# Kernel tuning notes

Hardware: AMD Instinct MI355X
Metric: run time of the kernel (lower is better)

Reference implementation:

```python
import jax, jax.numpy as jnp
import numpy as np

WS = 7            # cubic window
HEADS = 6
DIM = 96          # attention channel dim (concat of two half-streams)
CH = 48           # per-stream channels (dim // 2)
HID = 384         # int(dim * mlp_ratio)
N = WS ** 3       # 343 tokens per window
EPS = 1e-5


def _rel_pos_index():
    c = np.stack(np.meshgrid(np.arange(WS), np.arange(WS), np.arange(WS), indexing='ij')).reshape(3, -1)
    rel = (c[:, :, None] - c[:, None, :]).transpose(1, 2, 0) + (WS - 1)
    rel[:, :, 0] *= (2 * WS - 1) * (2 * WS - 1)
    rel[:, :, 1] *= (2 * WS - 1)
    return rel.sum(-1)  # (N, N) int

RPI = jnp.asarray(_rel_pos_index())


def _ln(x, g, b):
    m = x.mean(-1, keepdims=True)
    v = ((x - m) ** 2).mean(-1, keepdims=True)
    return (x - m) * jax.lax.rsqrt(v + EPS) * g + b


def _win_part(x):
    B, H, W, T, C = x.shape
    x = x.reshape(B, H // WS, WS, W // WS, WS, T // WS, WS, C)
    return x.transpose(0, 1, 3, 5, 2, 4, 6, 7).reshape(-1, WS, WS, WS, C)


def _win_rev(w, B, H, W, T):
    C = w.shape[-1]
    x = w.reshape(B, H // WS, W // WS, T // WS, WS, WS, WS, C)
    return x.transpose(0, 1, 4, 2, 5, 3, 6, 7).reshape(B, H, W, T, C)


def _chessboard(wa, wb, gd, gh, gw):
    C = wa.shape[-1]
    a = wa.reshape(gd, gh, gw, WS, WS, WS, C)
    b = wb.reshape(gd, gh, gw, WS, WS, WS, C)
    i = jnp.arange(gd)[:, None, None]
    j = jnp.arange(gh)[None, :, None]
    k = jnp.arange(gw)[None, None, :]
    m = (((i + j + k) % 2) == 0)[..., None, None, None, None]
    return (jnp.where(m, a, b).reshape(-1, WS, WS, WS, C),
            jnp.where(m, b, a).reshape(-1, WS, WS, WS, C))


def _attn(x, mask, rpb, qkv_w, qkv_b, proj_w, proj_b):
    B_, n, C = x.shape
    hd = C // HEADS
    qkv = (x @ qkv_w + qkv_b).reshape(B_, n, 3, HEADS, hd).transpose(2, 0, 3, 1, 4)
    q, k, v = qkv[0] * (hd ** -0.5), qkv[1], qkv[2]
    att = jnp.einsum('bhnd,bhmd->bhnm', q, k)
    att = att + rpb[RPI].transpose(2, 0, 1)[None]   # relative position bias gather
    att = att + mask[:, None]                        # shift mask; B_ == nW since B == 1
    att = jax.nn.softmax(att, axis=-1)
    out = jnp.einsum('bhnm,bhmd->bhnd', att, v).transpose(0, 2, 1, 3).reshape(B_, n, C)
    return out @ proj_w + proj_b


def _mlp(x, w1, b1, w2, b2):
    return jax.nn.gelu(x @ w1 + b1, approximate=False) @ w2 + b2


def _forward(x_a, x_b, mask_matrix, n1a_g, n1a_b, n1b_g, n1b_b,
             rpb_a, qkvw_a, qkvb_a, projw_a, projb_a,
             rpb_b, qkvw_b, qkvb_b, projw_b, projb_b,
             n2a_g, n2a_b, n2b_g, n2b_b,
             fc1w_a, fc1b_a, fc2w_a, fc2b_a, fc1w_b, fc1b_b, fc2w_b, fc2b_b,
             gw1, gw2, gb2, H, W, T):
    B, L, _ = x_a.shape
    sa0, sb0 = x_a, x_b
    a = _ln(x_a, n1a_g, n1a_b).reshape(B, H, W, T, CH)
    b = _ln(x_b, n1b_g, n1b_b).reshape(B, H, W, T, CH)
    # chessboard cross-stream shuffle of windows (shifted-window branch)
    ca, cb = _chessboard(_win_part(a), _win_part(b), H // WS, W // WS, T // WS)
    a_cr = _win_rev(ca, B, H, W, T)
    b_cr = _win_rev(cb, B, H, W, T)
    neg, pos, dims = (-3, -3, -3), (3, 3, 3), (1, 2, 3)
    sa, sb = jnp.roll(a, neg, dims), jnp.roll(b, neg, dims)
    sac, sbc = jnp.roll(a_cr, neg, dims), jnp.roll(b_cr, neg, dims)
    xa_w = _win_part(jnp.concatenate([sa, sbc], -1)).reshape(-1, N, DIM)
    xb_w = _win_part(jnp.concatenate([sb, sac], -1)).reshape(-1, N, DIM)
    oa = _attn(xa_w, mask_matrix, rpb_a, qkvw_a, qkvb_a, projw_a, projb_a)
    ob = _attn(xb_w, mask_matrix, rpb_b, qkvw_b, qkvb_b, projw_b, projb_b)
    oa = jnp.roll(_win_rev(oa.reshape(-1, WS, WS, WS, DIM), B, H, W, T), pos, dims)[..., :CH].reshape(B, L, CH)
    ob = jnp.roll(_win_rev(ob.reshape(-1, WS, WS, WS, DIM), B, H, W, T), pos, dims)[..., :CH].reshape(B, L, CH)
    x_a = sa0 + oa
    x_b = sb0 + ob
    x_a = x_a + _mlp(_ln(x_a, n2a_g, n2a_b), fc1w_a, fc1b_a, fc2w_a, fc2b_a)
    x_b = x_b + _mlp(_ln(x_b, n2b_g, n2b_b), fc1w_b, fc1b_b, fc2w_b, fc2b_b)
    g = jax.nn.sigmoid(jnp.maximum(x_a.mean(1) @ gw1, 0.0) @ gw2 + gb2)[:, :, None]  # (B,1,1)
    x_a = x_a + g * x_b
    return x_a, x_b


def setup_inputs():
    key = jax.random.key(0)
    ks = iter(jax.random.split(key, 24))
    H = W = T = 35
    L = H * W * T
    nW = (H // WS) * (W // WS) * (T // WS)
    p = lambda shape: jax.random.normal(next(ks), shape, jnp.float32) * 0.02
    d = {
        'x_a': jax.random.normal(next(ks), (1, L, CH), jnp.float32),
        'x_b': jax.random.normal(next(ks), (1, L, CH), jnp.float32),
        'mask_matrix': jax.random.normal(next(ks), (nW, N, N), jnp.float32),
        'n1a_g': jnp.ones((CH,), jnp.float32), 'n1a_b': jnp.zeros((CH,), jnp.float32),
        'n1b_g': jnp.ones((CH,), jnp.float32), 'n1b_b': jnp.zeros((CH,), jnp.float32),
        'rpb_a': p(((2 * WS - 1) ** 3, HEADS)),
        'qkvw_a': p((DIM, 3 * DIM)), 'qkvb_a': jnp.zeros((3 * DIM,), jnp.float32),
        'projw_a': p((DIM, DIM)), 'projb_a': jnp.zeros((DIM,), jnp.float32),
        'rpb_b': p(((2 * WS - 1) ** 3, HEADS)),
        'qkvw_b': p((DIM, 3 * DIM)), 'qkvb_b': jnp.zeros((3 * DIM,), jnp.float32),
        'projw_b': p((DIM, DIM)), 'projb_b': jnp.zeros((DIM,), jnp.float32),
        'n2a_g': jnp.ones((CH,), jnp.float32), 'n2a_b': jnp.zeros((CH,), jnp.float32),
        'n2b_g': jnp.ones((CH,), jnp.float32), 'n2b_b': jnp.zeros((CH,), jnp.float32),
        'fc1w_a': p((CH, HID)), 'fc1b_a': jnp.zeros((HID,), jnp.float32),
        'fc2w_a': p((HID, CH)), 'fc2b_a': jnp.zeros((CH,), jnp.float32),
        'fc1w_b': p((CH, HID)), 'fc1b_b': jnp.zeros((HID,), jnp.float32),
        'fc2w_b': p((HID, CH)), 'fc2b_b': jnp.zeros((CH,), jnp.float32),
        'gw1': p((CH, CH // 4)), 'gw2': p((CH // 4, 1)),
        'gb2': jnp.full((1,), -2.0, jnp.float32),
        'H': H, 'W': W, 'T': T,
    }
    return d


def reference(x_a, x_b, mask_matrix, n1a_g, n1a_b, n1b_g, n1b_b,
              rpb_a, qkvw_a, qkvb_a, projw_a, projb_a,
              rpb_b, qkvw_b, qkvb_b, projw_b, projb_b,
              n2a_g, n2a_b, n2b_g, n2b_b,
              fc1w_a, fc1b_a, fc2w_a, fc2b_a, fc1w_b, fc1b_b, fc2w_b, fc2b_b,
              gw1, gw2, gb2, H, W, T):
    return _forward(x_a, x_b, mask_matrix, n1a_g, n1a_b, n1b_g, n1b_b,
                    rpb_a, qkvw_a, qkvb_a, projw_a, projb_a,
                    rpb_b, qkvw_b, qkvb_b, projw_b, projb_b,
                    n2a_g, n2a_b, n2b_g, n2b_b,
                    fc1w_a, fc1b_a, fc2w_a, fc2b_a, fc1w_b, fc1b_b, fc2w_b, fc2b_b,
                    gw1, gw2, gb2, H, W, T)
```

## Files before the change

kernel.cpp:

```cpp
#include <hip/hip_runtime.h>
#include <hip/hip_fp16.h>

#define LQ    42875
#define NTOK  343
#define X1SZ  2058000

#define OFF_MEAN 0
#define OFF_QKV  36928
#define OFF_WF   12500000
#define QKV_BYTES_NEEDED 50400000ull

typedef _Float16 f16x8 __attribute__((ext_vector_type(8)));
typedef float f32x4 __attribute__((ext_vector_type(4)));
union B128 { uint4 u; f16x8 h; _Float16 e[8]; };

__device__ __forceinline__ int src_index(int w, int i, int& par) {
  int gi = w / 25, gj = (w / 5) % 5, gk = w % 5;
  int ph = i / 49, pw = (i / 7) % 7, pt = i % 7;
  int hs = gi * 7 + ph + 3; if (hs >= 35) hs -= 35;
  int wd = gj * 7 + pw + 3; if (wd >= 35) wd -= 35;
  int td = gk * 7 + pt + 3; if (td >= 35) td -= 35;
  par = ((hs / 7) + (wd / 7) + (td / 7)) & 1;
  return (hs * 35 + wd) * 35 + td;
}

__global__ __launch_bounds__(64) void k_init(float* __restrict__ ws) {
  if (threadIdx.x < 49) ws[threadIdx.x] = 0.f;
}

__global__ __launch_bounds__(256) void k_pack(
    const float* __restrict__ w1a, const float* __restrict__ w1b,
    const float* __restrict__ w2a, const float* __restrict__ w2b,
    const float* __restrict__ qwa, const float* __restrict__ qwb,
    float* __restrict__ ws) {
  int idx = blockIdx.x * 256 + threadIdx.x;
  if (idx >= 17664) return;
  uint4* WFB = (uint4*)(ws + OFF_WF);
  unsigned short h[8];
  uint4* dst;
  if (idx < 10752) {
    int s = idx / 5376, r = idx - s * 5376;
    uint4* WF = WFB + (size_t)s * 5376;
    if (r < 3072) {
      int jn = r / 128, t = r - jn * 128, kk = t / 64, lane = t - kk * 64;
      int q = lane >> 4, n = lane & 15;
      const float* w1 = s ? w1b : w1a;
      int j = jn * 16 + n;
#pragma unroll
      for (int e = 0; e < 8; e++) {
        int k = kk * 32 + q * 8 + e;
        float v = (k < 48) ? w1[k * 384 + j] : 0.f;
        h[e] = __half_as_ushort(__float2half(v));
      }
    } else {
      int rr = r - 3072;
      int kt = rr / 192, t = rr - kt * 192, cn = t / 64, lane = t - cn * 64;
      int q = lane >> 4, n = lane & 15;
      const float* w2 = s ? w2b : w2a;
      int c = cn * 16 + n;
#pragma unroll
      for (int e = 0; e < 8; e++) {
        int j = kt * 32 + q * 8 + e;
        h[e] = __half_as_ushort(__float2half(w2[j * 48 + c]));
      }
    }
    dst = WF + r;
  } else {
    int idx2 = idx - 10752;
    int s = idx2 / 3456, r = idx2 - s * 3456;
    int jn = r / 192, t = r - jn * 192, kk = t / 64, lane = t - kk * 64;
    int q = lane >> 4, n = lane & 15;
    const float* qw = s ? qwb : qwa;
    int j = jn * 16 + n;
#pragma unroll
    for (int e = 0; e < 8; e++) {
      int k = kk * 32 + q * 8 + e;
      h[e] = __half_as_ushort(__float2half(qw[k * 288 + j]));
    }
    dst = WFB + 10752 + (size_t)s * 3456 + r;
  }
  uint4 u;
  u.x = (unsigned)h[0] | ((unsigned)h[1] << 16);
  u.y = (unsigned)h[2] | ((unsigned)h[3] << 16);
  u.z = (unsigned)h[4] | ((unsigned)h[5] << 16);
  u.w = (unsigned)h[6] | ((unsigned)h[7] << 16);
  *dst = u;
}

__global__ __launch_bounds__(256) void k_qkv(
    const float* __restrict__ xa, const float* __restrict__ xb,
    const float* __restrict__ ga, const float* __restrict__ ba,
    const float* __restrict__ gb, const float* __restrict__ bb,
    const float* __restrict__ qba, const float* __restrict__ qbb,
    const float* __restrict__ ws, __half* __restrict__ qkvh) {
  __shared__ uint4 LDSB[2368];
  int s = blockIdx.z;
  int tid = threadIdx.x;
  int wid = tid >> 6, lane = tid & 63;
  int quad = lane >> 4, n15 = lane & 15;
  uint4* WR = LDSB + wid * 592;
  _Float16* th = (_Float16*)WR;
  int tbase = blockIdx.x * 64 + wid * 16;

  if (lane < 32) {
    int tt = lane & 15, which = lane >> 4;
    int t = tbase + tt;
    float v[48];
    bool wr = false, dup = false;
    if (t < LQ) {
      int w = t / 343, i = t - w * 343;
      int par; int src = src_index(w, i, par);
      const float* xr; const float* G; const float* B;
      bool doit;
      if (which == 0) { xr = (s ? xb : xa) + src * 48; G = s ? gb : ga; B = s ? bb : ba; doit = true; dup = (par == 1); }
      else            { xr = (s ? xa : xb) + src * 48; G = s ? ga : gb; B = s ? ba : bb; doit = (par == 0); }
      if (doit) {
        float sm = 0.f, sq = 0.f;
#pragma unroll
        for (int q4 = 0; q4 < 12; q4++) {
          float4 tv = ((const float4*)xr)[q4];
          v[4 * q4] = tv.x; v[4 * q4 + 1] = tv.y; v[4 * q4 + 2] = tv.z; v[4 * q4 + 3] = tv.w;
          sm += tv.x + tv.y + tv.z + tv.w;
          sq += tv.x * tv.x + tv.y * tv.y + tv.z * tv.z + tv.w * tv.w;
        }
        float m = sm * (1.f / 48.f);
        float r = rsqrtf(sq * (1.f / 48.f) - m * m + 1e-5f);
#pragma unroll
        for (int k = 0; k < 48; k++) v[k] = (v[k] - m) * r * G[k] + B[k];
        wr = true;
      }
    } else if (which == 0) {
#pragma unroll
      for (int k = 0; k < 48; k++) v[k] = 0.f;
      wr = true; dup = true;
    }
    if (wr) {
#pragma unroll
      for (int c6 = 0; c6 < 6; c6++) {
        unsigned short h[8];
#pragma unroll
        for (int e = 0; e < 8; e++) h[e] = __half_as_ushort(__float2half(v[c6 * 8 + e]));
        uint4 u;
        u.x = (unsigned)h[0] | ((unsigned)h[1] << 16);
        u.y = (unsigned)h[2] | ((unsigned)h[3] << 16);
        u.z = (unsigned)h[4] | ((unsigned)h[5] << 16);
        u.w = (unsigned)h[6] | ((unsigned)h[7] << 16);
        WR[(which * 6 + c6) * 16 + tt] = u;
        if (dup) WR[(6 + c6) * 16 + tt] = u;
      }
    }
  }

  B128 ax0, ax1, ax2;
  ax0.u = WR[(0 + quad) * 16 + n15];
  ax1.u = WR[(4 + quad) * 16 + n15];
  ax2.u = WR[(8 + quad) * 16 + n15];

  const uint4* QF = (const uint4*)(ws + OFF_WF) + 10752 + (size_t)s * 3456;
  const float* QB = s ? qbb : qba;
  const f32x4 ZC = {0.f, 0.f, 0.f, 0.f};

  for (int jn = 0; jn < 18; jn++) {
    B128 b0, b1, b2;
    b0.u = QF[(jn * 3 + 0) * 64 + lane];
    b1.u = QF[(jn * 3 + 1) * 64 + lane];
    b2.u = QF[(jn * 3 + 2) * 64 + lane];
    f32x4 c = __builtin_amdgcn_mfma_f32_16x16x32_f16(ax0.h, b0.h, ZC, 0, 0, 0);
    c = __builtin_amdgcn_mfma_f32_16x16x32_f16(ax1.h, b1.h, c, 0, 0, 0);
    c = __builtin_amdgcn_mfma_f32_16x16x32_f16(ax2.h, b2.h, c, 0, 0, 0);
    float bias = QB[jn * 16 + n15];
    float scale = (jn < 6) ? 0.25f : 1.0f;
#pragma unroll
    for (int r = 0; r < 4; r++)
      th[(quad * 4 + r) * 296 + jn * 16 + n15] = (_Float16)((c[r] + bias) * scale);
  }
  for (int e = lane; e < 576; e += 64) {
    int row = e / 36, cc = e - row * 36;
    int t = tbase + row;
    if (t < LQ)
      ((uint4*)qkvh)[(size_t)(s * LQ + t) * 36 + cc] = WR[row * 37 + cc];
  }
}

__global__ __launch_bounds__(256) void k_attn(
    const float* __restrict__ rpa, const float* __restrict__ rpbp,
    const float* __restrict__ mask, __half* __restrict__ qkvh) {
  int bid = blockIdx.x;
  int xcd = bid & 7, q8 = bid >> 3;
  int u = q8 / 12, inst = q8 - u * 12;
  int w = u * 8 + xcd;
  if (w >= 125) return;
  int s = inst & 1, h = inst >> 1;

  __shared__ uint4 FRAG[2368];
  __shared__ float rpbl[2197];
  uint4* Qf4 = FRAG;
  uint4* Kf4 = FRAG + 704;
  uint4* Vf4 = FRAG + 1408;
  uint4* Pb4 = FRAG + 2112;
  _Float16* Vfh = (_Float16*)(FRAG + 1408);
  _Float16* Pbh = (_Float16*)(FRAG + 2112);

  int tid = threadIdx.x;
  const uint4 Z4 = {0u, 0u, 0u, 0u};
  for (int e = tid; e < 2112; e += 256) FRAG[e] = Z4;
  const float* rp = s ? rpbp : rpa;
  for (int idx = tid; idx < 2197; idx += 256) rpbl[idx] = rp[idx * 6 + h];
  __syncthreads();

  size_t wbase = (size_t)((s * 125 + w) * NTOK) * 288;
  for (int i = tid; i < NTOK; i += 256) {
    const uint4* row = (const uint4*)(qkvh + wbase + (size_t)i * 288) + (h * 2);
    uint4 q0 = row[0], q1 = row[1];
    uint4 k0 = row[12], k1 = row[13];
    B128 v0, v1; v0.u = row[24]; v1.u = row[25];
    int n = i & 15, it = i >> 4;
    Qf4[it * 32 + n] = q0;
    Qf4[it * 32 + 16 + n] = q1;
    Kf4[it * 32 + n] = k0;
    Kf4[it * 32 + 16 + n] = k1;
    int vbase = ((i >> 5) * 64 + ((i >> 3) & 3) * 16) * 8 + (i & 7);
#pragma unroll
    for (int d = 0; d < 8; d++) {
      Vfh[vbase + d * 8] = v0.e[d];
      Vfh[vbase + (d + 8) * 8] = v1.e[d];
    }
  }
  __syncthreads();

  int wid = tid >> 6, lane = tid & 63;
  int quad = lane >> 4, n15 = lane & 15;
  const f32x4 ZC = {0.f, 0.f, 0.f, 0.f};
  __half* obh = qkvh;

  for (int it = wid; it < 22; it += 4) {
    int i0 = it * 16;
    const float* mr[4]; int basei[4];
#pragma unroll
    for (int r = 0; r < 4; r++) {
      int ir = i0 + quad * 4 + r; if (ir > 342) ir = 342;
      mr[r] = mask + (size_t)(w * NTOK + ir) * NTOK;
      basei[r] = (ir / 49) * 169 + ((ir / 7) % 7) * 13 + (ir % 7) + 1098;
    }
    B128 qbits; qbits.u = Qf4[it * 32 + ((quad & 1) << 4) + n15];
    if (quad >= 2) qbits.u = Z4;
    f32x4 acc = ZC;
    float ls[4] = {0.f, 0.f, 0.f, 0.f};

    float mcur[8], mnxt[8];
    {
      int ja = n15, jb = n15 + 16;
#pragma unroll
      for (int r = 0; r < 4; r++) { mcur[r] = mr[r][ja]; mcur[4 + r] = mr[r][jb]; }
    }
    for (int j32 = 0; j32 < 11; j32++) {
      if (j32 < 10) {
        int ja = (j32 + 1) * 32 + n15, jb = ja + 16;
        bool vb = jb < NTOK;
#pragma unroll
        for (int r = 0; r < 4; r++) {
          mnxt[r] = mr[r][ja];
          mnxt[4 + r] = vb ? mr[r][jb] : -1e30f;
        }
      }
      B128 kb0, kb1;
      kb0.u = Kf4[(j32 * 2) * 32 + ((quad & 1) << 4) + n15];
      kb1.u = Kf4[(j32 * 2 + 1) * 32 + ((quad & 1) << 4) + n15];
      if (quad >= 2) { kb0.u = Z4; kb1.u = Z4; }
      f32x4 s0 = __builtin_amdgcn_mfma_f32_16x16x32_f16(qbits.h, kb0.h, ZC, 0, 0, 0);
      f32x4 s1 = __builtin_amdgcn_mfma_f32_16x16x32_f16(qbits.h, kb1.h, ZC, 0, 0, 0);
      int j0 = j32 * 32 + n15;
      int j1 = j0 + 16;
      int bj0 = (j0 / 49) * 169 + ((j0 / 7) % 7) * 13 + (j0 % 7);
      int bj1 = (j1 < 343) ? (j1 / 49) * 169 + ((j1 / 7) % 7) * 13 + (j1 % 7) : 0;
      float p0[4], p1[4];
#pragma unroll
      for (int r = 0; r < 4; r++) {
        float b0 = mcur[r] + rpbl[basei[r] - bj0];
        float b1 = mcur[4 + r] + rpbl[basei[r] - bj1];
        p0[r] = __expf(s0[r] + b0);
        p1[r] = __expf(s1[r] + b1);
        ls[r] += p0[r] + p1[r];
      }
      int jj = n15 & 7;
      int ldA = ((n15 >> 3) * 16 + quad * 4) * 8 + jj + wid * 512;
      int ldB = ((2 + (n15 >> 3)) * 16 + quad * 4) * 8 + jj + wid * 512;
#pragma unroll
      for (int r = 0; r < 4; r++) {
        Pbh[ldA + r * 8] = (_Float16)p0[r];
        Pbh[ldB + r * 8] = (_Float16)p1[r];
      }
      B128 pb, vbits;
      pb.u = Pb4[wid * 64 + lane];
      vbits.u = Vf4[j32 * 64 + lane];
      acc = __builtin_amdgcn_mfma_f32_16x16x32_f16(pb.h, vbits.h, acc, 0, 0, 0);
#pragma unroll
      for (int e = 0; e < 8; e++) mcur[e] = mnxt[e];
    }
#pragma unroll
    for (int r = 0; r < 4; r++) {
      float v = ls[r];
      v += __shfl_xor(v, 1); v += __shfl_xor(v, 2);
      v += __shfl_xor(v, 4); v += __shfl_xor(v, 8);
      int ir = i0 + quad * 4 + r;
      if (ir < 343)
        obh[wbase + (size_t)ir * 288 + h * 16 + n15] = __float2half(acc[r] * (1.f / v));
    }
  }
}

__global__ __launch_bounds__(384) void k_proj(
    const __half* __restrict__ qkvh,
    const float* __restrict__ xa0, const float* __restrict__ xb0,
    const float* __restrict__ pwa, const float* __restrict__ pba,
    const float* __restrict__ pwb, const float* __restrict__ pbb,
    float* __restrict__ out) {
  int sw = blockIdx.x; int s = sw / 125, w = sw - s * 125;
  int i = threadIdx.x;
  if (i >= NTOK) return;
  const float* Wt = s ? pwb : pwa;
  const float* Bi = s ? pbb : pba;
  const uint4* orow = (const uint4*)(qkvh + (size_t)((s * 125 + w) * NTOK + i) * 288);
  float acc[48];
#pragma unroll
  for (int c = 0; c < 48; c++) acc[c] = 0.f;
#pragma unroll
  for (int k8 = 0; k8 < 12; k8++) {
    B128 ov; ov.u = orow[k8];
#pragma unroll
    for (int e = 0; e < 8; e++) {
      float x = (float)ov.e[e];
      const float* wr = Wt + (k8 * 8 + e) * 96;
#pragma unroll
      for (int c = 0; c < 48; c++) acc[c] = fmaf(x, wr[c], acc[c]);
    }
  }
  int par; int src = src_index(w, i, par);
  const float* x0 = (s ? xb0 : xa0) + src * 48;
  float* dst = out + s * X1SZ + src * 48;
#pragma unroll
  for (int q = 0; q < 12; q++) {
    float4 xv = ((const float4*)x0)[q];
    float4 o;
    o.x = xv.x + acc[4 * q + 0] + Bi[4 * q + 0];
    o.y = xv.y + acc[4 * q + 1] + Bi[4 * q + 1];
    o.z = xv.z + acc[4 * q + 2] + Bi[4 * q + 2];
    o.w = xv.w + acc[4 * q + 3] + Bi[4 * q + 3];
    ((float4*)dst)[q] = o;
  }
}

__global__ __launch_bounds__(256) void k_mlp(
    const float* __restrict__ g2a, const float* __restrict__ b2a,
    const float* __restrict__ g2b, const float* __restrict__ b2b,
    const float* __restrict__ fb1a, const float* __restrict__ fb2a,
    const float* __restrict__ fb1b, const float* __restrict__ fb2b,
    float* __restrict__ out, float* __restrict__ ws) {
  __shared__ uint4 Xf[512];
  __shared__ uint4 tbu[320];
  __shared__ float red[48];
  int s = blockIdx.z;
  int tid = threadIdx.x;
  int wid = tid >> 6, lane = tid & 63;
  int quad = lane >> 4, n15 = lane & 15;
  if (tid < 48) red[tid] = 0.f;
  __syncthreads();

  const float* B1 = s ? fb1b : fb1a;
  const float* B2 = s ? fb2b : fb2a;
  const uint4* W1F = (const uint4*)(ws + OFF_WF) + (size_t)s * 5376;
  const uint4* W2F = W1F + 3072;
  int tbase = blockIdx.x * 64 + wid * 16;
  float* outs = out + (size_t)s * X1SZ;

  if (lane < 16) {
    int t = tbase + lane;
    float v[48];
    if (t < LQ) {
      const float* row = outs + (size_t)t * 48;
      float sm = 0.f, sq = 0.f;
#pragma unroll
      for (int q4 = 0; q4 < 12; q4++) {
        float4 tv = ((const float4*)row)[q4];
        v[4 * q4] = tv.x; v[4 * q4 + 1] = tv.y; v[4 * q4 + 2] = tv.z; v[4 * q4 + 3] = tv.w;
        sm += tv.x + tv.y + tv.z + tv.w;
        sq += tv.x * tv.x + tv.y * tv.y + tv.z * tv.z + tv.w * tv.w;
      }
      float m = sm * (1.f / 48.f);
      float r = rsqrtf(sq * (1.f / 48.f) - m * m + 1e-5f);
      const float* G = s ? g2b : g2a;
      const float* B = s ? b2b : b2a;
#pragma unroll
      for (int k = 0; k < 48; k++) v[k] = (v[k] - m) * r * G[k] + B[k];
    } else {
#pragma unroll
      for (int k = 0; k < 48; k++) v[k] = 0.f;
    }
#pragma unroll
    for (int kc = 0; kc < 8; kc++) {
      uint4 u = {0u, 0u, 0u, 0u};
      if (kc < 6) {
        unsigned short h[8];
#pragma unroll
        for (int e = 0; e < 8; e++) h[e] = __half_as_ushort(__float2half(v[kc * 8 + e]));
        u.x = (unsigned)h[0] | ((unsigned)h[1] << 16);
        u.y = (unsigned)h[2] | ((unsigned)h[3] << 16);
        u.z = (unsigned)h[4] | ((unsigned)h[5] << 16);
        u.w = (unsigned)h[6] | ((unsigned)h[7] << 16);
      }
      Xf[wid * 128 + kc * 16 + lane] = u;
    }
  }

  _Float16* mytb = (_Float16*)(tbu + wid * 80);
  const uint4* mytb4 = tbu + wid * 80;
  const f32x4 ZC = {0.f, 0.f, 0.f, 0.f};
  f32x4 oacc[3] = {ZC, ZC, ZC};
  B128 ax0, ax1;
  ax0.u = Xf[wid * 128 + quad * 16 + n15];
  ax1.u = Xf[wid * 128 + (4 + quad) * 16 + n15];

  for (int kt = 0; kt < 12; kt++) {
    int jn0 = kt * 2, jn1 = jn0 + 1;
    B128 w0, w1, w2, w3;
    w0.u = W1F[jn0 * 128 + lane];
    w1.u = W1F[jn0 * 128 + 64 + lane];
    w2.u = W1F[jn1 * 128 + lane];
    w3.u = W1F[jn1 * 128 + 64 + lane];
    f32x4 a0 = __builtin_amdgcn_mfma_f32_16x16x32_f16(ax0.h, w0.h, ZC, 0, 0, 0);
    a0 = __builtin_amdgcn_mfma_f32_16x16x32_f16(ax1.h, w1.h, a0, 0, 0, 0);
    f32x4 a1 = __builtin_amdgcn_mfma_f32_16x16x32_f16(ax0.h, w2.h, ZC, 0, 0, 0);
    a1 = __builtin_amdgcn_mfma_f32_16x16x32_f16(ax1.h, w3.h, a1, 0, 0, 0);
    float bz0 = B1[jn0 * 16 + n15], bz1 = B1[jn1 * 16 + n15];
#pragma unroll
    for (int r = 0; r < 4; r++) {
      float h0 = a0[r] + bz0;
      h0 = 0.5f * h0 * (1.f + erff(h0 * 0.70710678118654752f));
      float h1 = a1[r] + bz1;
      h1 = 0.5f * h1 * (1.f + erff(h1 * 0.70710678118654752f));
      int rowb = (quad * 4 + r) * 40;
      mytb[rowb + n15] = (_Float16)h0;
      mytb[rowb + 16 + n15] = (_Float16)h1;
    }
    B128 pa; pa.u = mytb4[n15 * 5 + quad];
    B128 c0, c1, c2;
    c0.u = W2F[kt * 192 + lane];
    c1.u = W2F[kt * 192 + 64 + lane];
    c2.u = W2F[kt * 192 + 128 + lane];
    oacc[0] = __builtin_amdgcn_mfma_f32_16x16x32_f16(pa.h, c0.h, oacc[0], 0, 0, 0);
    oacc[1] = __builtin_amdgcn_mfma_f32_16x16x32_f16(pa.h, c1.h, oacc[1], 0, 0, 0);
    oacc[2] = __builtin_amdgcn_mfma_f32_16x16x32_f16(pa.h, c2.h, oacc[2], 0, 0, 0);
  }

  float b2v[3];
#pragma unroll
  for (int cn = 0; cn < 3; cn++) b2v[cn] = B2[cn * 16 + n15];
  float gsum[3] = {0.f, 0.f, 0.f};
#pragma unroll
  for (int r = 0; r < 4; r++) {
    int t = tbase + quad * 4 + r;
    bool val = t < LQ;
    float* orow = outs + (size_t)(val ? t : 0) * 48;
#pragma unroll
    for (int cn = 0; cn < 3; cn++) {
      float fin = 0.f;
      if (val) {
        fin = orow[cn * 16 + n15] + oacc[cn][r] + b2v[cn];
        orow[cn * 16 + n15] = fin;
      }
      gsum[cn] += fin;
    }
  }
  if (s == 0) {
#pragma unroll
    for (int cn = 0; cn < 3; cn++) {
      float v = gsum[cn];
      v += __shfl_xor(v, 16); v += __shfl_xor(v, 32);
      if (quad == 0) atomicAdd(&red[cn * 16 + n15], v);
    }
  }
  __syncthreads();
  if (s == 0 && tid < 48) atomicAdd(ws + OFF_MEAN + tid, red[tid]);
}

__global__ __launch_bounds__(64) void k_gate(
    const float* __restrict__ ws_mean, const float* __restrict__ gw1,
    const float* __restrict__ gw2, const float* __restrict__ gb2,
    float* __restrict__ g) {
  int j = threadIdx.x;
  float t = 0.f;
  if (j < 12) {
    for (int c = 0; c < 48; c++)
      t = fmaf(ws_mean[c] * (1.f / (float)LQ), gw1[c * 12 + j], t);
    t = fmaxf(t, 0.f) * gw2[j];
  }
  for (int off = 32; off > 0; off >>= 1) t += __shfl_down(t, off);
  if (j == 0) *g = 1.f / (1.f + __expf(-(t + gb2[0])));
}

__global__ __launch_bounds__(256) void k_gadd(float* __restrict__ out,
                                              const float* __restrict__ g) {
  int i = blockIdx.x * 256 + threadIdx.x;
  if (i >= X1SZ / 4) return;
  float gv = *g;
  float4* a = (float4*)out;
  const float4* b = (const float4*)(out + X1SZ);
  float4 x = a[i], y = b[i];
  x.x = fmaf(gv, y.x, x.x);
  x.y = fmaf(gv, y.y, x.y);
  x.z = fmaf(gv, y.z, x.z);
  x.w = fmaf(gv, y.w, x.w);
  a[i] = x;
}

extern "C" void kernel_launch(void* const* d_in, const int* in_sizes, int n_in,
                              void* d_out, int out_size, void* d_ws, size_t ws_size,
                              hipStream_t stream) {
  const float* xa    = (const float*)d_in[0];
  const float* xb    = (const float*)d_in[1];
  const float* mask  = (const float*)d_in[2];
  const float* n1ag  = (const float*)d_in[3];
  const float* n1ab  = (const float*)d_in[4];
  const float* n1bg  = (const float*)d_in[5];
  const float* n1bb  = (const float*)d_in[6];
  const float* rpba  = (const float*)d_in[7];
  const float* qkvwa = (const float*)d_in[8];
  const float* qkvba = (const float*)d_in[9];
  const float* pwa   = (const float*)d_in[10];
  const float* pba   = (const float*)d_in[11];
  const float* rpbb  = (const float*)d_in[12];
  const float* qkvwb = (const float*)d_in[13];
  const float* qkvbb = (const float*)d_in[14];
  const float* pwb   = (const float*)d_in[15];
  const float* pbb   = (const float*)d_in[16];
  const float* n2ag  = (const float*)d_in[17];
  const float* n2ab  = (const float*)d_in[18];
  const float* n2bg  = (const float*)d_in[19];
  const float* n2bb  = (const float*)d_in[20];
  const float* w1a   = (const float*)d_in[21];
  const float* fb1a  = (const float*)d_in[22];
  const float* w2a   = (const float*)d_in[23];
  const float* fb2a  = (const float*)d_in[24];
  const float* w1b   = (const float*)d_in[25];
  const float* fb1b  = (const float*)d_in[26];
  const float* w2b   = (const float*)d_in[27];
  const float* fb2b  = (const float*)d_in[28];
  const float* gw1   = (const float*)d_in[29];
  const float* gw2   = (const float*)d_in[30];
  const float* gb2   = (const float*)d_in[31];
  float* ws  = (float*)d_ws;
  float* out = (float*)d_out;

  if (ws_size < QKV_BYTES_NEEDED) return;
  __half* qkvh = (__half*)(ws + OFF_QKV);

  hipLaunchKernelGGL(k_init, dim3(1), dim3(64), 0, stream, ws);
  hipLaunchKernelGGL(k_pack, dim3(69), dim3(256), 0, stream,
                     w1a, w1b, w2a, w2b, qkvwa, qkvwb, ws);
  hipLaunchKernelGGL(k_qkv, dim3(670, 1, 2), dim3(256), 0, stream,
                     xa, xb, n1ag, n1ab, n1bg, n1bb,
                     qkvba, qkvbb, ws, qkvh);
  hipLaunchKernelGGL(k_attn, dim3(1536), dim3(256), 0, stream,
                     rpba, rpbb, mask, qkvh);
  hipLaunchKernelGGL(k_proj, dim3(250), dim3(384), 0, stream,
                     qkvh, xa, xb, pwa, pba, pwb, pbb, out);
  hipLaunchKernelGGL(k_mlp, dim3(670, 1, 2), dim3(256), 0, stream,
                     n2ag, n2ab, n2bg, n2bb,
                     fb1a, fb2a, fb1b, fb2b, out, ws);
  hipLaunchKernelGGL(k_gate, dim3(1), dim3(64), 0, stream,
                     ws + OFF_MEAN, gw1, gw2, gb2, ws + OFF_MEAN + 48);
  hipLaunchKernelGGL(k_gadd, dim3(2011), dim3(256), 0, stream,
                     out, ws + OFF_MEAN + 48);
}
```

Measured before the change: 439.9 us.

## Precompute dense relative-position bias matrix and swizzle P buffer in attention

New measurement: 458.8 us. +4.3%, slower.

```diff
diff --git a/kernel.cpp b/kernel.cpp
--- a/kernel.cpp
+++ b/kernel.cpp
@@ -8,7 +8,8 @@
 #define OFF_MEAN 0
 #define OFF_QKV  36928
 #define OFF_WF   12500000
-#define QKV_BYTES_NEEDED 50400000ull
+#define OFF_RPB  12600000
+#define QKV_BYTES_NEEDED 56100000ull
 
 typedef _Float16 f16x8 __attribute__((ext_vector_type(8)));
 typedef float f32x4 __attribute__((ext_vector_type(4)));
@@ -87,6 +88,20 @@
   *dst = u;
 }
 
+__global__ __launch_bounds__(256) void k_rpb(
+    const float* __restrict__ rpa, const float* __restrict__ rpbp,
+    float* __restrict__ ws) {
+  int sh = blockIdx.y;
+  int s = sh / 6, h = sh - s * 6;
+  int idx = blockIdx.x * 256 + threadIdx.x;
+  if (idx >= 117649) return;
+  int ir = idx / 343, j = idx - ir * 343;
+  int bi = (ir / 49) * 169 + ((ir / 7) % 7) * 13 + (ir % 7) + 1098;
+  int bj = (j / 49) * 169 + ((j / 7) % 7) * 13 + (j % 7);
+  const float* rp = s ? rpbp : rpa;
+  ws[OFF_RPB + (size_t)sh * 117649 + idx] = rp[(bi - bj) * 6 + h];
+}
+
 __global__ __launch_bounds__(256) void k_qkv(
     const float* __restrict__ xa, const float* __restrict__ xb,
     const float* __restrict__ ga, const float* __restrict__ ba,
@@ -183,7 +198,7 @@
 }
 
 __global__ __launch_bounds__(256) void k_attn(
-    const float* __restrict__ rpa, const float* __restrict__ rpbp,
+    const float* __restrict__ rpbmat,
     const float* __restrict__ mask, __half* __restrict__ qkvh) {
   int bid = blockIdx.x;
   int xcd = bid & 7, q8 = bid >> 3;
@@ -193,7 +208,6 @@
   int s = inst & 1, h = inst >> 1;
 
   __shared__ uint4 FRAG[2368];
-  __shared__ float rpbl[2197];
   uint4* Qf4 = FRAG;
   uint4* Kf4 = FRAG + 704;
   uint4* Vf4 = FRAG + 1408;
@@ -204,8 +218,6 @@
   int tid = threadIdx.x;
   const uint4 Z4 = {0u, 0u, 0u, 0u};
   for (int e = tid; e < 2112; e += 256) FRAG[e] = Z4;
-  const float* rp = s ? rpbp : rpa;
-  for (int idx = tid; idx < 2197; idx += 256) rpbl[idx] = rp[idx * 6 + h];
   __syncthreads();
 
   size_t wbase = (size_t)((s * 125 + w) * NTOK) * 288;
@@ -230,28 +242,45 @@
 
   int wid = tid >> 6, lane = tid & 63;
   int quad = lane >> 4, n15 = lane & 15;
+  int jj = n15 & 7, hi = n15 >> 3;
   const f32x4 ZC = {0.f, 0.f, 0.f, 0.f};
   __half* obh = qkvh;
+  const float* rbase = rpbmat + (size_t)(s * 6 + h) * 117649;
+
+  int pA[4], pB[4];
+#pragma unroll
+  for (int r = 0; r < 4; r++) {
+    int ra = hi * 16 + quad * 4 + r;
+    int rb = (2 + hi) * 16 + quad * 4 + r;
+    ra ^= (ra >> 3) & 7;
+    rb ^= (rb >> 3) & 7;
+    pA[r] = wid * 512 + ra * 8 + jj;
+    pB[r] = wid * 512 + rb * 8 + jj;
+  }
+  int rdrow = wid * 64 + (lane ^ ((lane >> 3) & 7));
 
   for (int it = wid; it < 22; it += 4) {
     int i0 = it * 16;
-    const float* mr[4]; int basei[4];
+    const float* mr[4]; const float* rr[4];
 #pragma unroll
     for (int r = 0; r < 4; r++) {
       int ir = i0 + quad * 4 + r; if (ir > 342) ir = 342;
       mr[r] = mask + (size_t)(w * NTOK + ir) * NTOK;
-      basei[r] = (ir / 49) * 169 + ((ir / 7) % 7) * 13 + (ir % 7) + 1098;
+      rr[r] = rbase + ir * NTOK;
     }
     B128 qbits; qbits.u = Qf4[it * 32 + ((quad & 1) << 4) + n15];
     if (quad >= 2) qbits.u = Z4;
     f32x4 acc = ZC;
     float ls[4] = {0.f, 0.f, 0.f, 0.f};
 
-    float mcur[8], mnxt[8];
+    float mcur[8], mnxt[8], rcur[8], rnxt[8];
     {
       int ja = n15, jb = n15 + 16;
 #pragma unroll
-      for (int r = 0; r < 4; r++) { mcur[r] = mr[r][ja]; mcur[4 + r] = mr[r][jb]; }
+      for (int r = 0; r < 4; r++) {
+        mcur[r] = mr[r][ja]; mcur[4 + r] = mr[r][jb];
+        rcur[r] = rr[r][ja]; rcur[4 + r] = rr[r][jb];
+      }
     }
     for (int j32 = 0; j32 < 11; j32++) {
       if (j32 < 10) {
@@ -261,6 +290,8 @@
         for (int r = 0; r < 4; r++) {
           mnxt[r] = mr[r][ja];
           mnxt[4 + r] = vb ? mr[r][jb] : -1e30f;
+          rnxt[r] = rr[r][ja];
+          rnxt[4 + r] = vb ? rr[r][jb] : 0.f;
         }
       }
       B128 kb0, kb1;
@@ -269,33 +300,24 @@
       if (quad >= 2) { kb0.u = Z4; kb1.u = Z4; }
       f32x4 s0 = __builtin_amdgcn_mfma_f32_16x16x32_f16(qbits.h, kb0.h, ZC, 0, 0, 0);
       f32x4 s1 = __builtin_amdgcn_mfma_f32_16x16x32_f16(qbits.h, kb1.h, ZC, 0, 0, 0);
-      int j0 = j32 * 32 + n15;
-      int j1 = j0 + 16;
-      int bj0 = (j0 / 49) * 169 + ((j0 / 7) % 7) * 13 + (j0 % 7);
-      int bj1 = (j1 < 343) ? (j1 / 49) * 169 + ((j1 / 7) % 7) * 13 + (j1 % 7) : 0;
       float p0[4], p1[4];
 #pragma unroll
       for (int r = 0; r < 4; r++) {
-        float b0 = mcur[r] + rpbl[basei[r] - bj0];
-        float b1 = mcur[4 + r] + rpbl[basei[r] - bj1];
-        p0[r] = __expf(s0[r] + b0);
-        p1[r] = __expf(s1[r] + b1);
+        p0[r] = __expf(s0[r] + mcur[r] + rcur[r]);
+        p1[r] = __expf(s1[r] + mcur[4 + r] + rcur[4 + r]);
         ls[r] += p0[r] + p1[r];
       }
-      int jj = n15 & 7;
-      int ldA = ((n15 >> 3) * 16 + quad * 4) * 8 + jj + wid * 512;
-      int ldB = ((2 + (n15 >> 3)) * 16 + quad * 4) * 8 + jj + wid * 512;
 #pragma unroll
       for (int r = 0; r < 4; r++) {
-        Pbh[ldA + r * 8] = (_Float16)p0[r];
-        Pbh[ldB + r * 8] = (_Float16)p1[r];
+        Pbh[pA[r]] = (_Float16)p0[r];
+        Pbh[pB[r]] = (_Float16)p1[r];
       }
       B128 pb, vbits;
-      pb.u = Pb4[wid * 64 + lane];
+      pb.u = Pb4[rdrow];
       vbits.u = Vf4[j32 * 64 + lane];
       acc = __builtin_amdgcn_mfma_f32_16x16x32_f16(pb.h, vbits.h, acc, 0, 0, 0);
 #pragma unroll
-      for (int e = 0; e < 8; e++) mcur[e] = mnxt[e];
+      for (int e = 0; e < 8; e++) { mcur[e] = mnxt[e]; rcur[e] = rnxt[e]; }
     }
 #pragma unroll
     for (int r = 0; r < 4; r++) {
@@ -557,11 +579,13 @@
   hipLaunchKernelGGL(k_init, dim3(1), dim3(64), 0, stream, ws);
   hipLaunchKernelGGL(k_pack, dim3(69), dim3(256), 0, stream,
                      w1a, w1b, w2a, w2b, qkvwa, qkvwb, ws);
+  hipLaunchKernelGGL(k_rpb, dim3(460, 12), dim3(256), 0, stream,
+                     rpba, rpbb, ws);
   hipLaunchKernelGGL(k_qkv, dim3(670, 1, 2), dim3(256), 0, stream,
                      xa, xb, n1ag, n1ab, n1bg, n1bb,
                      qkvba, qkvbb, ws, qkvh);
   hipLaunchKernelGGL(k_attn, dim3(1536), dim3(256), 0, stream,
-                     rpba, rpbb, mask, qkvh);
+                     ws + OFF_RPB, mask, qkvh);
   hipLaunchKernelGGL(k_proj, dim3(250), dim3(384), 0, stream,
                      qkvh, xa, xb, pwa, pba, pwb, pbb, out);
   hipLaunchKernelGGL(k_mlp, dim3(670, 1, 2), dim3(256), 0, stream,
```
